# Kernel optimization log

Measured on AMD Instinct MI355X. Metric: run time of the kernel, lower is better.

The kernel has to match this reference:

```python
import jax, jax.numpy as jnp
import numpy as np

N_NODES = 100000
N_EDGES = 3200000
D_IN = 128
D_OUT = 128
LN_EPS = 1e-5


def setup_inputs() -> dict:
    key = jax.random.key(0)
    k1, k2, k3, k4 = jax.random.split(key, 4)
    x = jax.random.normal(k1, (N_NODES, D_IN), dtype=jnp.float32)
    edge_index = jax.random.randint(k2, (2, N_EDGES), 0, N_NODES, dtype=jnp.int64)
    # GCNConv weight (glorot-ish scale) and bias
    W = jax.random.normal(k3, (D_IN, D_OUT), dtype=jnp.float32) / np.sqrt(D_IN)
    b = jnp.zeros((D_OUT,), dtype=jnp.float32)
    # LayerNorm params
    gamma = jnp.ones((D_OUT,), dtype=jnp.float32)
    beta = jnp.zeros((D_OUT,), dtype=jnp.float32)
    return {"x": x, "edge_index": edge_index, "W": W, "b": b, "gamma": gamma, "beta": beta}


def reference(x, edge_index, W, b, gamma, beta):
    # GCNConv: add self-loops, symmetric degree normalization, aggregate, add bias.
    N = x.shape[0]
    self_loops = jnp.arange(N, dtype=edge_index.dtype)
    row = jnp.concatenate([edge_index[0], self_loops])  # destination
    col = jnp.concatenate([edge_index[1], self_loops])  # source
    deg = jax.ops.segment_sum(jnp.ones(row.shape[0], x.dtype), row, num_segments=N)
    dinv = jnp.where(deg > 0, jax.lax.rsqrt(deg), 0.0)
    norm = dinv[row] * dinv[col]                         # [E+N]
    xw = x @ W                                           # [N, D_OUT]
    msg = norm[:, None] * xw[col]                        # gather + scale [E+N, D_OUT]
    agg = jax.ops.segment_sum(msg, row, num_segments=N) + b  # scatter-add
    # LayerNorm over feature dim
    mu = jnp.mean(agg, axis=-1, keepdims=True)
    var = jnp.mean(jnp.square(agg - mu), axis=-1, keepdims=True)
    h = (agg - mu) * jax.lax.rsqrt(var + LN_EPS) * gamma + beta
    # ReLU; Dropout is identity in eval mode
    return jax.nn.relu(h)
```

## Files before the change

kernel.cpp:

```cpp
#include <hip/hip_runtime.h>

#define N_NODES 100000
#define N_EDGES 3200000
#define D 128
#define NB 782
#define BCAP 5120
#define STAGE 16

__device__ __forceinline__ float bf2f(unsigned short u) {
  return __uint_as_float(((unsigned)u) << 16);
}
__device__ __forceinline__ unsigned short f2bf(float f) {
  unsigned u = __float_as_uint(f);
  u += 0x7FFF + ((u >> 16) & 1);
  return (unsigned short)(u >> 16);
}

__global__ void detect_kernel(const int* __restrict__ ei32, int* __restrict__ flag) {
  __shared__ int anynz;
  if (threadIdx.x == 0) anynz = 0;
  __syncthreads();
  int v = 0;
  for (int i = threadIdx.x; i < 2048; i += 256) v |= ei32[2 * i + 1];
  if (v) atomicOr(&anynz, 1);
  __syncthreads();
  if (threadIdx.x == 0) *flag = (anynz == 0) ? 1 : 0;
}

__global__ void zero_kernel(int* __restrict__ p, int n) {
  int i = blockIdx.x * blockDim.x + threadIdx.x;
  if (i < n) p[i] = 0;
}

__global__ __launch_bounds__(256) void partition_kernel(const void* __restrict__ edges,
                                                        const int* __restrict__ flag,
                                                        int* __restrict__ gcur,
                                                        unsigned int* __restrict__ bstore) {
  __shared__ unsigned int stage[NB][STAGE];
  __shared__ int scnt[NB];
  const bool is64 = (*flag != 0);
  for (int i = threadIdx.x; i < NB; i += 256) scnt[i] = 0;
  __syncthreads();
  int gstride = gridDim.x * blockDim.x;
  for (int base = blockIdx.x * blockDim.x; base < N_EDGES; base += gstride) {
    int e = base + threadIdx.x;
    if (e < N_EDGES) {
      int r, c;
      if (is64) {
        r = (int)((const long long*)edges)[e];
        c = (int)((const long long*)edges)[N_EDGES + e];
      } else {
        r = ((const int*)edges)[e];
        c = ((const int*)edges)[N_EDGES + e];
      }
      int b = r >> 7;
      unsigned ent = ((unsigned)(r & 127) << 17) | (unsigned)c;
      int pos = atomicAdd(&scnt[b], 1);
      if (pos < STAGE) {
        stage[b][pos] = ent;
      } else {
        int gp = atomicAdd(&gcur[b], 1);
        if (gp < BCAP) bstore[(size_t)b * BCAP + gp] = ent;
      }
    }
    __syncthreads();
    for (int b = threadIdx.x; b < NB; b += 256) {
      if (scnt[b] >= STAGE) {
        int gp = atomicAdd(&gcur[b], STAGE);
        if (gp + STAGE <= BCAP) {
          uint4* dst = (uint4*)&bstore[(size_t)b * BCAP + gp];
          uint4* src = (uint4*)&stage[b][0];
          dst[0] = src[0];
          dst[1] = src[1];
          dst[2] = src[2];
          dst[3] = src[3];
        } else {
          for (int k = 0; k < STAGE; k++)
            if (gp + k < BCAP) bstore[(size_t)b * BCAP + gp + k] = stage[b][k];
        }
        scnt[b] = 0;
      }
    }
    __syncthreads();
  }
  for (int b = threadIdx.x; b < NB; b += 256) {
    int n = scnt[b];
    if (n > STAGE) n = STAGE;
    if (n > 0) {
      int gp = atomicAdd(&gcur[b], n);
      for (int k = 0; k < n; k++)
        if (gp + k < BCAP) bstore[(size_t)b * BCAP + gp + k] = stage[b][k];
    }
  }
}

__global__ __launch_bounds__(256) void bucket_kernel(const int* __restrict__ gcur,
                                                     unsigned int* __restrict__ bstore,
                                                     int* __restrict__ cnt,
                                                     int* __restrict__ start,
                                                     float* __restrict__ dinv) {
  __shared__ unsigned int ent[BCAP];
  __shared__ int lcnt[128];
  __shared__ int s[128];
  __shared__ int loffs[128];
  int b = blockIdx.x, tid = threadIdx.x;
  size_t base = (size_t)b * BCAP;
  int m = gcur[b];
  if (m > BCAP) m = BCAP;
  int nodes = N_NODES - b * 128;
  if (nodes > 128) nodes = 128;

  for (int i = tid; i < m; i += 256) ent[i] = bstore[base + i];
  if (tid < 128) lcnt[tid] = 0;
  __syncthreads();
  for (int i = tid; i < m; i += 256) atomicAdd(&lcnt[ent[i] >> 17], 1);
  __syncthreads();
  if (tid < 128) s[tid] = lcnt[tid];
  __syncthreads();
#pragma unroll
  for (int off = 1; off < 128; off <<= 1) {
    int v = (tid < 128 && tid >= off) ? s[tid - off] : 0;
    __syncthreads();
    if (tid < 128) s[tid] += v;
    __syncthreads();
  }
  if (tid < nodes) {
    int st = (tid == 0) ? 0 : s[tid - 1];
    int node = b * 128 + tid;
    start[node] = (int)base + st;
    cnt[node] = lcnt[tid];
    dinv[node] = rsqrtf((float)(lcnt[tid] + 1));
    loffs[tid] = st;
  }
  __syncthreads();
  for (int i = tid; i < m; i += 256) {
    unsigned u = ent[i];
    int lr = u >> 17;
    int pos = atomicAdd(&loffs[lr], 1);
    bstore[base + pos] = u & 0x1FFFF;
  }
}

__global__ __launch_bounds__(256) void gemm_kernel(const float* __restrict__ x,
                                                   const float* __restrict__ W,
                                                   const float* __restrict__ dinv,
                                                   unsigned short* __restrict__ y) {
  __shared__ float xs[32][132];
  __shared__ float ws[32][128];
  int tid = threadIdx.x;
  int row0 = blockIdx.x * 32;
#pragma unroll
  for (int i = 0; i < 4; i++) {
    int idx = tid + i * 256;
    int m = idx >> 5, c4 = (idx & 31) << 2;
    *(float4*)&xs[m][c4] = *(const float4*)(x + (size_t)(row0 + m) * D + c4);
  }
  float acc[4][4] = {};
  int tx = tid & 31, ty = tid >> 5;
  for (int k0 = 0; k0 < 128; k0 += 32) {
#pragma unroll
    for (int i = 0; i < 4; i++) {
      int idx = tid + i * 256;
      int kk = idx >> 5, c4 = (idx & 31) << 2;
      *(float4*)&ws[kk][c4] = *(const float4*)(W + (size_t)(k0 + kk) * D + c4);
    }
    __syncthreads();
#pragma unroll
    for (int k = 0; k < 32; k += 4) {
      float4 a0 = *(float4*)&xs[ty * 4 + 0][k0 + k];
      float4 a1 = *(float4*)&xs[ty * 4 + 1][k0 + k];
      float4 a2 = *(float4*)&xs[ty * 4 + 2][k0 + k];
      float4 a3 = *(float4*)&xs[ty * 4 + 3][k0 + k];
      float4 w0 = *(float4*)&ws[k + 0][tx * 4];
      float4 w1 = *(float4*)&ws[k + 1][tx * 4];
      float4 w2 = *(float4*)&ws[k + 2][tx * 4];
      float4 w3 = *(float4*)&ws[k + 3][tx * 4];
#define ROWFMA(i, ai)                                              \
      acc[i][0] += ai.x * w0.x + ai.y * w1.x + ai.z * w2.x + ai.w * w3.x; \
      acc[i][1] += ai.x * w0.y + ai.y * w1.y + ai.z * w2.y + ai.w * w3.y; \
      acc[i][2] += ai.x * w0.z + ai.y * w1.z + ai.z * w2.z + ai.w * w3.z; \
      acc[i][3] += ai.x * w0.w + ai.y * w1.w + ai.z * w2.w + ai.w * w3.w;
      ROWFMA(0, a0)
      ROWFMA(1, a1)
      ROWFMA(2, a2)
      ROWFMA(3, a3)
#undef ROWFMA
    }
    __syncthreads();
  }
#pragma unroll
  for (int i = 0; i < 4; i++) {
    int row = row0 + ty * 4 + i;
    float di = dinv[row];
    unsigned short h0 = f2bf(di * acc[i][0]);
    unsigned short h1 = f2bf(di * acc[i][1]);
    unsigned short h2 = f2bf(di * acc[i][2]);
    unsigned short h3 = f2bf(di * acc[i][3]);
    uint2 pk;
    pk.x = (unsigned)h0 | ((unsigned)h1 << 16);
    pk.y = (unsigned)h2 | ((unsigned)h3 << 16);
    *(uint2*)(y + (size_t)row * D + tx * 4) = pk;
  }
}

__global__ __launch_bounds__(256) void agg_ln_kernel(
    const unsigned short* __restrict__ y, const unsigned int* __restrict__ csr,
    const int* __restrict__ start, const int* __restrict__ cnt,
    const float* __restrict__ dinv, const float* __restrict__ bias,
    const float* __restrict__ gamma, const float* __restrict__ beta,
    float* __restrict__ out) {
  int wid = threadIdx.x >> 6, lane = threadIdx.x & 63;
  int node = blockIdx.x * 4 + wid;
  if (node >= N_NODES) return;
  const unsigned short* yl = y + 2 * lane;
  int s = start[node];
  int n = cnt[node];
  ushort2 sv = *(const ushort2*)(yl + (size_t)node * D);
  float acc0 = bf2f(sv.x), acc1 = bf2f(sv.y);
  for (int j = 0; j < n; j += 64) {
    int m = n - j;
    if (m > 64) m = 64;
    int cj = (j + lane < n) ? (int)csr[s + j + lane] : 0;
    int t = 0;
    for (; t + 3 < m; t += 4) {
      int c0 = __shfl(cj, t);
      int c1 = __shfl(cj, t + 1);
      int c2 = __shfl(cj, t + 2);
      int c3 = __shfl(cj, t + 3);
      ushort2 v0 = *(const ushort2*)(yl + (size_t)c0 * D);
      ushort2 v1 = *(const ushort2*)(yl + (size_t)c1 * D);
      ushort2 v2 = *(const ushort2*)(yl + (size_t)c2 * D);
      ushort2 v3 = *(const ushort2*)(yl + (size_t)c3 * D);
      acc0 += bf2f(v0.x) + bf2f(v1.x) + bf2f(v2.x) + bf2f(v3.x);
      acc1 += bf2f(v0.y) + bf2f(v1.y) + bf2f(v2.y) + bf2f(v3.y);
    }
    for (; t < m; t++) {
      int c0 = __shfl(cj, t);
      ushort2 v0 = *(const ushort2*)(yl + (size_t)c0 * D);
      acc0 += bf2f(v0.x);
      acc1 += bf2f(v0.y);
    }
  }
  float di = dinv[node];
  float v0 = fmaf(di, acc0, bias[2 * lane]);
  float v1 = fmaf(di, acc1, bias[2 * lane + 1]);
  float sum = v0 + v1;
#pragma unroll
  for (int msk = 1; msk <= 32; msk <<= 1) sum += __shfl_xor(sum, msk);
  float mu = sum * (1.0f / 128.0f);
  float d0 = v0 - mu, d1 = v1 - mu;
  float sq = d0 * d0 + d1 * d1;
#pragma unroll
  for (int msk = 1; msk <= 32; msk <<= 1) sq += __shfl_xor(sq, msk);
  float rstd = rsqrtf(sq * (1.0f / 128.0f) + 1e-5f);
  float h0 = fmaxf(fmaf(d0 * rstd, gamma[2 * lane], beta[2 * lane]), 0.0f);
  float h1 = fmaxf(fmaf(d1 * rstd, gamma[2 * lane + 1], beta[2 * lane + 1]), 0.0f);
  float2 o;
  o.x = h0;
  o.y = h1;
  *(float2*)(out + (size_t)node * D + 2 * lane) = o;
}

extern "C" void kernel_launch(void* const* d_in, const int* in_sizes, int n_in,
                              void* d_out, int out_size, void* d_ws, size_t ws_size,
                              hipStream_t stream) {
  const float* x = (const float*)d_in[0];
  const void* edges = d_in[1];
  const float* W = (const float*)d_in[2];
  const float* b = (const float*)d_in[3];
  const float* gamma = (const float*)d_in[4];
  const float* beta = (const float*)d_in[5];
  float* out = (float*)d_out;

  char* w = (char*)d_ws;
  size_t off = 0;
  auto take = [&](size_t bytes) {
    size_t r = off;
    off += (bytes + 255) & ~(size_t)255;
    return r;
  };
  int* flag = (int*)(w + take(256));
  int* gcur = (int*)(w + take((size_t)NB * 4));
  int* cnt = (int*)(w + take((size_t)N_NODES * 4));
  int* start = (int*)(w + take((size_t)N_NODES * 4));
  float* dinv = (float*)(w + take((size_t)N_NODES * 4));
  unsigned int* bstore = (unsigned int*)(w + take((size_t)NB * BCAP * 4));
  unsigned short* y = (unsigned short*)(w + take((size_t)N_NODES * D * 2));

  detect_kernel<<<1, 256, 0, stream>>>((const int*)edges, flag);
  zero_kernel<<<(NB + 255) / 256, 256, 0, stream>>>(gcur, NB);
  partition_kernel<<<768, 256, 0, stream>>>(edges, flag, gcur, bstore);
  bucket_kernel<<<NB, 256, 0, stream>>>(gcur, bstore, cnt, start, dinv);
  gemm_kernel<<<N_NODES / 32, 256, 0, stream>>>(x, W, dinv, y);
  agg_ln_kernel<<<(N_NODES + 3) / 4, 256, 0, stream>>>(y, bstore, start, cnt, dinv, b, gamma,
                                                       beta, out);
}
```

Baseline: 352.9 us.

## Use bf16 MFMA for feature GEMM and gather two neighbors per wave step

Replaces the fp32 FMA tiled GEMM with a bf16 MFMA 16x16x32 kernel. W is pre-transposed and converted to bf16 once per call, and x is converted to bf16 while it is staged in shared memory. The aggregation kernel splits each wave into two halves that handle alternate neighbors with 8-byte loads, then combines the halves with a cross-lane shuffle before LayerNorm. This cuts GEMM compute cost and issues more independent gathers per step, at the cost of rounding x to bf16 and an extra tiny kernel launch.

```diff
diff --git a/kernel.cpp b/kernel.cpp
--- a/kernel.cpp
+++ b/kernel.cpp
@@ -7,6 +7,9 @@
 #define BCAP 5120
 #define STAGE 16
 
+typedef __attribute__((ext_vector_type(8))) short bf16x8;
+typedef __attribute__((ext_vector_type(4))) float f32x4;
+
 __device__ __forceinline__ float bf2f(unsigned short u) {
   return __uint_as_float(((unsigned)u) << 16);
 }
@@ -30,6 +33,17 @@
 __global__ void zero_kernel(int* __restrict__ p, int n) {
   int i = blockIdx.x * blockDim.x + threadIdx.x;
   if (i < n) p[i] = 0;
+}
+
+__global__ void prep_w_kernel(const float* __restrict__ W, unsigned short* __restrict__ wTg) {
+  int t = threadIdx.x;
+  int c = t >> 1, h = t & 1;
+  for (int k0 = h * 64; k0 < h * 64 + 64; k0 += 8) {
+    unsigned short tmp[8];
+#pragma unroll
+    for (int j = 0; j < 8; j++) tmp[j] = f2bf(W[(k0 + j) * D + c]);
+    *(uint4*)(wTg + c * D + k0) = *(uint4*)tmp;
+  }
 }
 
 __global__ __launch_bounds__(256) void partition_kernel(const void* __restrict__ edges,
@@ -141,65 +155,65 @@
   }
 }
 
-__global__ __launch_bounds__(256) void gemm_kernel(const float* __restrict__ x,
-                                                   const float* __restrict__ W,
-                                                   const float* __restrict__ dinv,
-                                                   unsigned short* __restrict__ y) {
-  __shared__ float xs[32][132];
-  __shared__ float ws[32][128];
+__global__ __launch_bounds__(256) void gemm_mfma_kernel(const float* __restrict__ x,
+                                                        const unsigned short* __restrict__ wTg,
+                                                        const float* __restrict__ dinv,
+                                                        unsigned short* __restrict__ y) {
+  __shared__ unsigned short xs[64 * 136];
+  __shared__ unsigned short wls[128 * 136];
   int tid = threadIdx.x;
-  int row0 = blockIdx.x * 32;
-#pragma unroll
-  for (int i = 0; i < 4; i++) {
-    int idx = tid + i * 256;
-    int m = idx >> 5, c4 = (idx & 31) << 2;
-    *(float4*)&xs[m][c4] = *(const float4*)(x + (size_t)(row0 + m) * D + c4);
-  }
-  float acc[4][4] = {};
-  int tx = tid & 31, ty = tid >> 5;
-  for (int k0 = 0; k0 < 128; k0 += 32) {
+  int row0 = blockIdx.x * 64;
+  {
+    int c = tid >> 1, h = tid & 1;
+    const uint4* src = (const uint4*)(wTg + c * D + h * 64);
+    uint4* dst = (uint4*)(wls + c * 136 + h * 64);
+#pragma unroll
+    for (int i = 0; i < 8; i++) dst[i] = src[i];
+  }
+  {
+    int rx = tid >> 2, q = tid & 3;
+    int r = row0 + rx;
+    if (r > N_NODES - 1) r = N_NODES - 1;
+    const float4* src = (const float4*)(x + (size_t)r * D + q * 32);
+    uint4* dst = (uint4*)(xs + rx * 136 + q * 32);
 #pragma unroll
     for (int i = 0; i < 4; i++) {
-      int idx = tid + i * 256;
-      int kk = idx >> 5, c4 = (idx & 31) << 2;
-      *(float4*)&ws[kk][c4] = *(const float4*)(W + (size_t)(k0 + kk) * D + c4);
-    }
-    __syncthreads();
-#pragma unroll
-    for (int k = 0; k < 32; k += 4) {
-      float4 a0 = *(float4*)&xs[ty * 4 + 0][k0 + k];
-      float4 a1 = *(float4*)&xs[ty * 4 + 1][k0 + k];
-      float4 a2 = *(float4*)&xs[ty * 4 + 2][k0 + k];
-      float4 a3 = *(float4*)&xs[ty * 4 + 3][k0 + k];
-      float4 w0 = *(float4*)&ws[k + 0][tx * 4];
-      float4 w1 = *(float4*)&ws[k + 1][tx * 4];
-      float4 w2 = *(float4*)&ws[k + 2][tx * 4];
-      float4 w3 = *(float4*)&ws[k + 3][tx * 4];
-#define ROWFMA(i, ai)                                              \
-      acc[i][0] += ai.x * w0.x + ai.y * w1.x + ai.z * w2.x + ai.w * w3.x; \
-      acc[i][1] += ai.x * w0.y + ai.y * w1.y + ai.z * w2.y + ai.w * w3.y; \
-      acc[i][2] += ai.x * w0.z + ai.y * w1.z + ai.z * w2.z + ai.w * w3.z; \
-      acc[i][3] += ai.x * w0.w + ai.y * w1.w + ai.z * w2.w + ai.w * w3.w;
-      ROWFMA(0, a0)
-      ROWFMA(1, a1)
-      ROWFMA(2, a2)
-      ROWFMA(3, a3)
-#undef ROWFMA
-    }
-    __syncthreads();
-  }
-#pragma unroll
-  for (int i = 0; i < 4; i++) {
-    int row = row0 + ty * 4 + i;
-    float di = dinv[row];
-    unsigned short h0 = f2bf(di * acc[i][0]);
-    unsigned short h1 = f2bf(di * acc[i][1]);
-    unsigned short h2 = f2bf(di * acc[i][2]);
-    unsigned short h3 = f2bf(di * acc[i][3]);
-    uint2 pk;
-    pk.x = (unsigned)h0 | ((unsigned)h1 << 16);
-    pk.y = (unsigned)h2 | ((unsigned)h3 << 16);
-    *(uint2*)(y + (size_t)row * D + tx * 4) = pk;
+      float4 fa = src[2 * i], fb = src[2 * i + 1];
+      uint4 p;
+      p.x = (unsigned)f2bf(fa.x) | ((unsigned)f2bf(fa.y) << 16);
+      p.y = (unsigned)f2bf(fa.z) | ((unsigned)f2bf(fa.w) << 16);
+      p.z = (unsigned)f2bf(fb.x) | ((unsigned)f2bf(fb.y) << 16);
+      p.w = (unsigned)f2bf(fb.z) | ((unsigned)f2bf(fb.w) << 16);
+      dst[i] = p;
+    }
+  }
+  __syncthreads();
+  int w = tid >> 6, l = tid & 63;
+  int g = l >> 4, ln = l & 15;
+  bf16x8 af[4];
+#pragma unroll
+  for (int kt = 0; kt < 4; kt++)
+    af[kt] = *(const bf16x8*)(xs + (w * 16 + ln) * 136 + kt * 32 + g * 8);
+  int rbase = row0 + w * 16 + 4 * g;
+  float dv[4];
+#pragma unroll
+  for (int j = 0; j < 4; j++) {
+    int r = rbase + j;
+    dv[j] = dinv[r < N_NODES ? r : N_NODES - 1];
+  }
+#pragma unroll
+  for (int ct = 0; ct < 8; ct++) {
+    f32x4 acc = {0.f, 0.f, 0.f, 0.f};
+#pragma unroll
+    for (int kt = 0; kt < 4; kt++) {
+      bf16x8 bf = *(const bf16x8*)(wls + (ct * 16 + ln) * 136 + kt * 32 + g * 8);
+      acc = __builtin_amdgcn_mfma_f32_16x16x32_bf16(af[kt], bf, acc, 0, 0, 0);
+    }
+#pragma unroll
+    for (int j = 0; j < 4; j++) {
+      int r = rbase + j;
+      if (r < N_NODES) y[(size_t)r * D + ct * 16 + ln] = f2bf(dv[j] * acc[j]);
+    }
   }
 }
 
@@ -212,53 +226,82 @@
   int wid = threadIdx.x >> 6, lane = threadIdx.x & 63;
   int node = blockIdx.x * 4 + wid;
   if (node >= N_NODES) return;
-  const unsigned short* yl = y + 2 * lane;
+  int half = lane >> 5, hl = lane & 31;
   int s = start[node];
   int n = cnt[node];
-  ushort2 sv = *(const ushort2*)(yl + (size_t)node * D);
-  float acc0 = bf2f(sv.x), acc1 = bf2f(sv.y);
+  float a0 = 0.f, a1 = 0.f, a2 = 0.f, a3 = 0.f;
   for (int j = 0; j < n; j += 64) {
     int m = n - j;
     if (m > 64) m = 64;
     int cj = (j + lane < n) ? (int)csr[s + j + lane] : 0;
     int t = 0;
-    for (; t + 3 < m; t += 4) {
-      int c0 = __shfl(cj, t);
-      int c1 = __shfl(cj, t + 1);
-      int c2 = __shfl(cj, t + 2);
-      int c3 = __shfl(cj, t + 3);
-      ushort2 v0 = *(const ushort2*)(yl + (size_t)c0 * D);
-      ushort2 v1 = *(const ushort2*)(yl + (size_t)c1 * D);
-      ushort2 v2 = *(const ushort2*)(yl + (size_t)c2 * D);
-      ushort2 v3 = *(const ushort2*)(yl + (size_t)c3 * D);
-      acc0 += bf2f(v0.x) + bf2f(v1.x) + bf2f(v2.x) + bf2f(v3.x);
-      acc1 += bf2f(v0.y) + bf2f(v1.y) + bf2f(v2.y) + bf2f(v3.y);
-    }
-    for (; t < m; t++) {
-      int c0 = __shfl(cj, t);
-      ushort2 v0 = *(const ushort2*)(yl + (size_t)c0 * D);
-      acc0 += bf2f(v0.x);
-      acc1 += bf2f(v0.y);
-    }
-  }
+    for (; t + 7 < m; t += 8) {
+      int e0 = __shfl(cj, t + half);
+      int e1 = __shfl(cj, t + 2 + half);
+      int e2 = __shfl(cj, t + 4 + half);
+      int e3 = __shfl(cj, t + 6 + half);
+      ushort4 v0 = *(const ushort4*)(y + (size_t)e0 * D + hl * 4);
+      ushort4 v1 = *(const ushort4*)(y + (size_t)e1 * D + hl * 4);
+      ushort4 v2 = *(const ushort4*)(y + (size_t)e2 * D + hl * 4);
+      ushort4 v3 = *(const ushort4*)(y + (size_t)e3 * D + hl * 4);
+      a0 += bf2f(v0.x) + bf2f(v1.x) + bf2f(v2.x) + bf2f(v3.x);
+      a1 += bf2f(v0.y) + bf2f(v1.y) + bf2f(v2.y) + bf2f(v3.y);
+      a2 += bf2f(v0.z) + bf2f(v1.z) + bf2f(v2.z) + bf2f(v3.z);
+      a3 += bf2f(v0.w) + bf2f(v1.w) + bf2f(v2.w) + bf2f(v3.w);
+    }
+    for (; t + 1 < m; t += 2) {
+      int e0 = __shfl(cj, t + half);
+      ushort4 v0 = *(const ushort4*)(y + (size_t)e0 * D + hl * 4);
+      a0 += bf2f(v0.x);
+      a1 += bf2f(v0.y);
+      a2 += bf2f(v0.z);
+      a3 += bf2f(v0.w);
+    }
+    if (t < m) {
+      int e0 = __shfl(cj, t);
+      if (half == 0) {
+        ushort4 v0 = *(const ushort4*)(y + (size_t)e0 * D + hl * 4);
+        a0 += bf2f(v0.x);
+        a1 += bf2f(v0.y);
+        a2 += bf2f(v0.z);
+        a3 += bf2f(v0.w);
+      }
+    }
+  }
+  a0 += __shfl_xor(a0, 32);
+  a1 += __shfl_xor(a1, 32);
+  a2 += __shfl_xor(a2, 32);
+  a3 += __shfl_xor(a3, 32);
+  ushort4 sv = *(const ushort4*)(y + (size_t)node * D + hl * 4);
+  a0 += bf2f(sv.x);
+  a1 += bf2f(sv.y);
+  a2 += bf2f(sv.z);
+  a3 += bf2f(sv.w);
   float di = dinv[node];
-  float v0 = fmaf(di, acc0, bias[2 * lane]);
-  float v1 = fmaf(di, acc1, bias[2 * lane + 1]);
-  float sum = v0 + v1;
+  float4 bi = *(const float4*)(bias + hl * 4);
+  float v0 = fmaf(di, a0, bi.x);
+  float v1 = fmaf(di, a1, bi.y);
+  float v2 = fmaf(di, a2, bi.z);
+  float v3 = fmaf(di, a3, bi.w);
+  float sum = v0 + v1 + v2 + v3;
 #pragma unroll
   for (int msk = 1; msk <= 32; msk <<= 1) sum += __shfl_xor(sum, msk);
-  float mu = sum * (1.0f / 128.0f);
-  float d0 = v0 - mu, d1 = v1 - mu;
-  float sq = d0 * d0 + d1 * d1;
+  float mu = sum * (1.0f / 256.0f);
+  float d0 = v0 - mu, d1 = v1 - mu, d2 = v2 - mu, d3 = v3 - mu;
+  float sq = d0 * d0 + d1 * d1 + d2 * d2 + d3 * d3;
 #pragma unroll
   for (int msk = 1; msk <= 32; msk <<= 1) sq += __shfl_xor(sq, msk);
-  float rstd = rsqrtf(sq * (1.0f / 128.0f) + 1e-5f);
-  float h0 = fmaxf(fmaf(d0 * rstd, gamma[2 * lane], beta[2 * lane]), 0.0f);
-  float h1 = fmaxf(fmaf(d1 * rstd, gamma[2 * lane + 1], beta[2 * lane + 1]), 0.0f);
-  float2 o;
-  o.x = h0;
-  o.y = h1;
-  *(float2*)(out + (size_t)node * D + 2 * lane) = o;
+  float rstd = rsqrtf(sq * (1.0f / 256.0f) + 1e-5f);
+  float4 ga = *(const float4*)(gamma + hl * 4);
+  float4 be = *(const float4*)(beta + hl * 4);
+  if (half == 0) {
+    float4 o;
+    o.x = fmaxf(fmaf(d0 * rstd, ga.x, be.x), 0.0f);
+    o.y = fmaxf(fmaf(d1 * rstd, ga.y, be.y), 0.0f);
+    o.z = fmaxf(fmaf(d2 * rstd, ga.z, be.z), 0.0f);
+    o.w = fmaxf(fmaf(d3 * rstd, ga.w, be.w), 0.0f);
+    *(float4*)(out + (size_t)node * D + hl * 4) = o;
+  }
 }
 
 extern "C" void kernel_launch(void* const* d_in, const int* in_sizes, int n_in,
@@ -284,14 +327,16 @@
   int* cnt = (int*)(w + take((size_t)N_NODES * 4));
   int* start = (int*)(w + take((size_t)N_NODES * 4));
   float* dinv = (float*)(w + take((size_t)N_NODES * 4));
+  unsigned short* wTg = (unsigned short*)(w + take((size_t)D * D * 2));
   unsigned int* bstore = (unsigned int*)(w + take((size_t)NB * BCAP * 4));
   unsigned short* y = (unsigned short*)(w + take((size_t)N_NODES * D * 2));
 
   detect_kernel<<<1, 256, 0, stream>>>((const int*)edges, flag);
   zero_kernel<<<(NB + 255) / 256, 256, 0, stream>>>(gcur, NB);
+  prep_w_kernel<<<1, 256, 0, stream>>>(W, wTg);
   partition_kernel<<<768, 256, 0, stream>>>(edges, flag, gcur, bstore);
   bucket_kernel<<<NB, 256, 0, stream>>>(gcur, bstore, cnt, start, dinv);
-  gemm_kernel<<<N_NODES / 32, 256, 0, stream>>>(x, W, dinv, y);
+  gemm_mfma_kernel<<<(N_NODES + 63) / 64, 256, 0, stream>>>(x, wTg, dinv, y);
   agg_ln_kernel<<<(N_NODES + 3) / 4, 256, 0, stream>>>(y, bstore, start, cnt, dinv, b, gamma,
                                                        beta, out);
 }
```

Measured after the change: 328.8 us. 6.8% less time.
